# Optimization experiments

Hardware: AMD Instinct MI355X
Metric: run time of the kernel (lower is better)

## Reference

```python
import jax, jax.numpy as jnp
import numpy as np

N_HEADS = 8

def setup_inputs() -> dict:
    key = jax.random.key(0)
    ks = jax.random.split(key, 7)
    B, S, D = 4, 2048, 512
    s = 1.0 / np.sqrt(D)
    return {
        "input_Q": jax.random.normal(ks[0], (B, S, D), jnp.float32),
        "input_K": jax.random.normal(ks[1], (B, S, D), jnp.float32),
        "input_V": jax.random.normal(ks[2], (B, S, D), jnp.float32),
        "W_Q": jax.random.normal(ks[3], (D, D), jnp.float32) * s,
        "W_K": jax.random.normal(ks[4], (D, D), jnp.float32) * s,
        "W_V": jax.random.normal(ks[5], (D, D), jnp.float32) * s,
        "W_O": jax.random.normal(ks[6], (D, D), jnp.float32) * s,
    }

def reference(input_Q, input_K, input_V, W_Q, W_K, W_V, W_O):
    B, Sq, D = input_Q.shape
    Sk = input_K.shape[1]
    H = N_HEADS
    d_k = D // H
    # torch nn.Linear(bias=False): y = x @ W.T
    def proj(x, W):
        return (x @ W.T).reshape(B, -1, H, d_k).transpose(0, 2, 1, 3)  # [B,H,S,dk]
    Q = proj(input_Q, W_Q)
    K = proj(input_K, W_K)
    V = proj(input_V, W_V)
    scale = 1.0 / jnp.sqrt(jnp.float32(d_k))
    scores = jnp.einsum("bhqd,bhkd->bhqk", Q, K) * scale  # [B,H,Sq,Sk]
    # TriangularCausalMask: mask strict upper triangle with -inf
    causal = jnp.tril(jnp.ones((Sq, Sk), dtype=bool))
    scores = jnp.where(causal[None, None], scores, -jnp.inf)
    attn = jax.nn.softmax(scores, axis=-1)
    context = jnp.einsum("bhqk,bhkd->bhqd", attn, V)
    context = context.transpose(0, 2, 1, 3).reshape(B, Sq, D)
    return context @ W_O.T
```

## Files before the change

kernel.cpp:

```cpp
#include <hip/hip_runtime.h>
#include <hip/hip_bf16.h>
#include <math.h>

#define B_  4
#define S_  2048
#define D_  512
#define H_  8
#define DK_ 64
#define M_  (B_ * S_)

using bf16   = __bf16;
using bf16x4 = __bf16 __attribute__((ext_vector_type(4)));
using bf16x8 = __bf16 __attribute__((ext_vector_type(8)));
using f32x4  = float __attribute__((ext_vector_type(4)));

#define MFMA16(a, b, c) __builtin_amdgcn_mfma_f32_16x16x32_bf16((a), (b), (c), 0, 0, 0)
#define EXP2(x) exp2f(x)

typedef __attribute__((address_space(3))) void       lds_void;
typedef const __attribute__((address_space(1))) void gbl_void;

__device__ __forceinline__ void async16(const bf16* g, bf16* lds) {
    __builtin_amdgcn_global_load_lds((gbl_void*)g, (lds_void*)lds, 16, 0, 0);
}

__device__ __forceinline__ bf16x8 ldg8(const bf16* p) {
    return *reinterpret_cast<const bf16x8*>(p);
}

__device__ __forceinline__ size_t fragbase(int g, int k0, int kk, int t) {
    return ((((size_t)(g * 8 + k0) * 2 + kk) * 4 + t) * 64) * 8;
}

__global__ __launch_bounds__(256) void cvt_w(
    const float* __restrict__ w0, const float* __restrict__ w1,
    const float* __restrict__ w2, const float* __restrict__ w3,
    bf16* __restrict__ dst)
{
    const int w    = blockIdx.x * 4 + (threadIdx.x >> 6);
    const int lane = threadIdx.x & 63;
    const int lg = lane >> 4, lc = lane & 15;
    const int seg = w >> 9;
    const int c   = w & 511;
    const float* src = (seg == 0) ? w0 : (seg == 1) ? w1 : (seg == 2) ? w2 : w3;
    const size_t dbase = (size_t)seg << 18;
    const int g = c >> 6, k0 = (c >> 3) & 7, kk = (c >> 2) & 1, t = c & 3;
    const size_t soff = ((size_t)(g * 64 + t * 16 + lc) << 9) + k0 * 64 + kk * 32 + lg * 8;
    f32x4 a = *reinterpret_cast<const f32x4*>(src + soff);
    f32x4 b = *reinterpret_cast<const f32x4*>(src + soff + 4);
    bf16x8 r;
    #pragma unroll
    for (int j = 0; j < 4; ++j) { r[j] = (bf16)a[j]; r[j + 4] = (bf16)b[j]; }
    *reinterpret_cast<bf16x8*>(dst + dbase + ((size_t)c << 9) + (size_t)lane * 8) = r;
}

__global__ __launch_bounds__(256, 3) void gemm_qkv(
    const float* __restrict__ x0, const float* __restrict__ x1,
    const float* __restrict__ x2, const bf16* __restrict__ Wf,
    bf16* __restrict__ qkv)
{
    const int bx  = blockIdx.x;
    const int xcd = bx & 7;
    const int idx = bx >> 3;
    const int mt  = xcd + 8 * (idx & 7);
    const int rest = idx >> 3;
    const int nt  = rest & 3;
    const int z   = rest >> 2;

    const float* X  = (z == 0) ? x0 : (z == 1) ? x1 : x2;
    const bf16*  Wz = Wf + (size_t)z * D_ * D_;
    const bool vz = (z == 2);

    const int lane = threadIdx.x & 63;
    const int wave = threadIdx.x >> 6;
    const int lc = lane & 15;
    const int lg = lane >> 4;
    const int aIdx = wave >> 1;
    const int bIdx = wave & 1;

    __shared__ bf16 Wb[2][4096];
    __shared__ bf16 Xb[2][4096];

    const int tid  = threadIdx.x;
    const int xc   = tid >> 5;
    const int xgx  = xc >> 2, xt = xc & 3;
    const int sub  = tid & 31;
    const int l0   = 2 * sub;
    const int xrow0 = (2 * mt + xgx) * 64 + xt * 16 + (l0 & 15);
    const int xcolg = (l0 >> 4) * 8;

    auto issueX = [&](int s, f32x4* r) {
        const int col = (s >> 1) * 64 + (s & 1) * 32 + xcolg;
        const float* p0 = X + (size_t)xrow0 * 512 + col;
        r[0] = *reinterpret_cast<const f32x4*>(p0);
        r[1] = *reinterpret_cast<const f32x4*>(p0 + 4);
        r[2] = *reinterpret_cast<const f32x4*>(p0 + 512);
        r[3] = *reinterpret_cast<const f32x4*>(p0 + 516);
    };
    auto issueW = [&](int s) {
        const int k0 = s >> 1, kk = s & 1;
        bf16* wd = Wb[s & 1];
        #pragma unroll
        for (int i = 0; i < 2; ++i) {
            const int c = wave * 2 + i;
            const int gx = c >> 2, t = c & 3;
            async16(Wz + fragbase(2 * nt + gx, k0, kk, t) + (size_t)lane * 8,
                    wd + (gx * 4 + t) * 512 + (size_t)lane * 8);
        }
    };
    auto writeX = [&](int s, const f32x4* r) {
        bf16* xd = Xb[s & 1];
        bf16x8 v0, v1;
        #pragma unroll
        for (int j = 0; j < 4; ++j) {
            v0[j] = (bf16)r[0][j]; v0[j + 4] = (bf16)r[1][j];
            v1[j] = (bf16)r[2][j]; v1[j + 4] = (bf16)r[3][j];
        }
        *reinterpret_cast<bf16x8*>(xd + xc * 512 + l0 * 8)       = v0;
        *reinterpret_cast<bf16x8*>(xd + xc * 512 + (l0 + 1) * 8) = v1;
    };

    f32x4 acc[4][4] = {};

    {
        f32x4 xr[4];
        issueX(0, xr); issueW(0);
        writeX(0, xr);
        __syncthreads();
    }

    for (int s = 0; s < 16; ++s) {
        f32x4 xn[4];
        if (s < 15) { issueX(s + 1, xn); issueW(s + 1); }

        const bf16* wb = Wb[s & 1];
        const bf16* xb = Xb[s & 1];
        const bf16* ap = (vz ? xb : wb) + aIdx * 2048;
        const bf16* bp = (vz ? wb : xb) + bIdx * 2048;
        bf16x8 af[4], bfm[4];
        #pragma unroll
        for (int t = 0; t < 4; ++t) {
            af[t]  = ldg8(ap + t * 512 + (size_t)lane * 8);
            bfm[t] = ldg8(bp + t * 512 + (size_t)lane * 8);
        }
        #pragma unroll
        for (int mi = 0; mi < 4; ++mi)
            #pragma unroll
            for (int ni = 0; ni < 4; ++ni)
                acc[mi][ni] = MFMA16(af[mi], bfm[ni], acc[mi][ni]);

        if (s < 15) writeX(s + 1, xn);
        __syncthreads();
    }

    const int gA = (vz ? 2 * mt : 2 * nt) + aIdx;
    const int gB = (vz ? 2 * nt : 2 * mt) + bIdx;

    if (z < 2) {
        bf16* Y = qkv + (size_t)z * M_ * D_;
        const float sc = (z == 0) ? 0.125f * 1.4426950408889634f : 1.0f;
        #pragma unroll
        for (int mi = 0; mi < 4; ++mi)
            #pragma unroll
            for (int ni = 0; ni < 4; ++ni) {
                const int d = gA * 64 + mi * 16 + lg * 4;
                const int s = gB * 64 + ni * 16 + lc;
                bf16x4 v;
                #pragma unroll
                for (int r = 0; r < 4; ++r) v[r] = (bf16)(acc[mi][ni][r] * sc);
                const size_t oidx =
                    ((((size_t)(s >> 11) * H_ + (d >> 6)) * S_
                      + (s & (S_ - 1))) << 6) + (d & 63);
                *reinterpret_cast<bf16x4*>(&Y[oidx]) = v;
            }
    } else {
        bf16* Y = qkv + (size_t)2 * M_ * D_;
        #pragma unroll
        for (int mi = 0; mi < 4; ++mi)
            #pragma unroll
            for (int ni = 0; ni < 4; ++ni) {
                const int s = gA * 64 + mi * 16 + lg * 4;
                const int d = gB * 64 + ni * 16 + lc;
                bf16x4 v;
                #pragma unroll
                for (int r = 0; r < 4; ++r) v[r] = (bf16)acc[mi][ni][r];
                const size_t oidx =
                    ((((size_t)(s >> 11)) * H_ + (d >> 6)) << 17)
                    + (size_t)(d & 63) * S_ + (s & (S_ - 1));
                *reinterpret_cast<bf16x4*>(&Y[oidx]) = v;
            }
    }
}

__global__ __launch_bounds__(256) void gemm_out(
    const bf16* __restrict__ CtxF, const bf16* __restrict__ WoF,
    float* __restrict__ out)
{
    const int bx  = blockIdx.x;
    const int xcd = bx & 7;
    const int idx = bx >> 3;
    const int mt  = xcd + 8 * (idx & 15);
    const int nt  = idx >> 4;

    const int lane = threadIdx.x & 63;
    const int wave = threadIdx.x >> 6;
    const int lc = lane & 15;
    const int lg = lane >> 4;
    const int gA = 2 * nt + (wave >> 1);
    const int tA = (wave & 1) * 2;
    const int gB = mt;

    __shared__ bf16 Ab[3][4096];
    __shared__ bf16 Bb[3][2048];

    auto stage = [&](int s) {
        const int k0 = s >> 1, kk = s & 1;
        bf16* ad = Ab[s % 3];
        bf16* bd = Bb[s % 3];
        #pragma unroll
        for (int i = 0; i < 3; ++i) {
            const int c = wave * 3 + i;
            if (c < 8) {
                const int gx = c >> 2, t = c & 3;
                async16(WoF + fragbase(2 * nt + gx, k0, kk, t) + (size_t)lane * 8,
                        ad + (gx * 4 + t) * 512 + (size_t)lane * 8);
            } else {
                const int t = c - 8;
                async16(CtxF + fragbase(gB, k0, kk, t) + (size_t)lane * 8,
                        bd + t * 512 + (size_t)lane * 8);
            }
        }
    };

    f32x4 acc[2][4] = {};

    stage(0); stage(1);

    for (int s = 0; s < 16; ++s) {
        if (s + 1 < 16) asm volatile("s_waitcnt vmcnt(3)" ::: "memory");
        else            asm volatile("s_waitcnt vmcnt(0)" ::: "memory");
        __builtin_amdgcn_s_barrier();
        if (s + 2 < 16) stage(s + 2);

        const bf16* ab = Ab[s % 3] + (wave >> 1) * 2048;
        const bf16* bb = Bb[s % 3];
        bf16x8 af[2], bfm[4];
        #pragma unroll
        for (int ai = 0; ai < 2; ++ai)
            af[ai] = ldg8(ab + (tA + ai) * 512 + (size_t)lane * 8);
        #pragma unroll
        for (int t = 0; t < 4; ++t)
            bfm[t] = ldg8(bb + t * 512 + (size_t)lane * 8);
        #pragma unroll
        for (int ai = 0; ai < 2; ++ai)
            #pragma unroll
            for (int ni = 0; ni < 4; ++ni)
                acc[ai][ni] = MFMA16(af[ai], bfm[ni], acc[ai][ni]);
    }

    #pragma unroll
    for (int ai = 0; ai < 2; ++ai)
        #pragma unroll
        for (int ni = 0; ni < 4; ++ni) {
            const int d = gA * 64 + (tA + ai) * 16 + lg * 4;
            const int s = gB * 64 + ni * 16 + lc;
            *reinterpret_cast<f32x4*>(&out[(size_t)s * D_ + d]) = acc[ai][ni];
        }
}

__device__ __forceinline__ bf16x8 pfrag(const f32x4 a, const f32x4 b) {
    union U4 { bf16x4 v; unsigned int u[2]; };
    U4 pa, pb;
    #pragma unroll
    for (int r = 0; r < 4; ++r) { pa.v[r] = (bf16)a[r]; pb.v[r] = (bf16)b[r]; }
    auto r0 = __builtin_amdgcn_permlane16_swap(pa.u[0], pb.u[0], false, false);
    auto r1 = __builtin_amdgcn_permlane16_swap(pa.u[1], pb.u[1], false, false);
    union U8 { unsigned int u[4]; bf16x8 v; } out;
    out.u[0] = r0[0]; out.u[1] = r1[0]; out.u[2] = r0[1]; out.u[3] = r1[1];
    return out.v;
}

__global__ __launch_bounds__(512, 4) void attn(
    const bf16* __restrict__ QKV, bf16* __restrict__ CtxF)
{
    const int bx = blockIdx.x;
    const int bh = (bx & 7) * 4 + ((bx >> 3) & 3);
    const int pi = bx >> 5;
    const int b = bh >> 3, h = bh & 7;
    const size_t plane = (size_t)S_ * DK_;
    const bf16* Q  = QKV + (size_t)bh * plane;
    const bf16* Kp = QKV + (size_t)(B_ * H_) * plane + (size_t)bh * plane;
    const bf16* Vt = QKV + 2 * (size_t)(B_ * H_) * plane + (size_t)bh * plane;

    const int lane = threadIdx.x & 63;
    const int wave = threadIdx.x >> 6;
    const int wv   = wave & 3;
    const int half = wave >> 2;
    const int lc = lane & 15;
    const int lg = lane >> 4;
    const int sg = ((lg & 1) << 1) | (lg >> 1);
    const int srow = wv * 16 + lc;
    const int mrow = wv * 16 + lc;

    __shared__ bf16 Ks[4][64 * 64];
    __shared__ bf16 Vs[4][64 * 64];

    const int lo = pi;
    const int hi = 31 - pi;
    const int myq = half ? lo : hi;

    const int qR = myq * 64 + mrow;
    bf16x8 qf0 = ldg8(Q + (size_t)qR * DK_ + lg * 8);
    bf16x8 qf1 = ldg8(Q + (size_t)qR * DK_ + 32 + lg * 8);

    f32x4 accO[4] = {};
    float li = 0.f;

    auto stage = [&](int n) {
        const int kn = n * 64;
        if (half == 0) {
            bf16* kd = Ks[n & 3];
            #pragma unroll
            for (int i = 0; i < 2; ++i) {
                const int kc = i * 4 + lg;
                async16(Kp + (size_t)(kn + srow) * DK_ + kc * 8,
                        kd + (i * 256 + wv * 64) * 8);
            }
        } else {
            bf16* vd = Vs[n & 3];
            #pragma unroll
            for (int i = 0; i < 2; ++i) {
                const int kcv = i * 4 + sg;
                async16(Vt + (size_t)srow * S_ + kn + kcv * 8,
                        vd + (i * 256 + wv * 64) * 8);
            }
        }
    };

    stage(0); stage(1); stage(2);

    for (int j = 0; j <= hi; ++j) {
        if (j + 2 <= hi)      asm volatile("s_waitcnt vmcnt(4)" ::: "memory");
        else if (j + 1 <= hi) asm volatile("s_waitcnt vmcnt(2)" ::: "memory");
        else                  asm volatile("s_waitcnt vmcnt(0)" ::: "memory");
        __builtin_amdgcn_s_barrier();
        if (j + 3 <= hi) stage(j + 3);

        if (j <= myq) {
            const bf16* ks = Ks[j & 3];
            const bf16* vs = Vs[j & 3];

            bf16x8 kf0[4], kf1[4], vf0[4], vf1[4];
            #pragma unroll
            for (int t = 0; t < 4; ++t) {
                kf0[t] = ldg8(&ks[(t * 64 + lane) * 8]);
                kf1[t] = ldg8(&ks[(256 + t * 64 + lane) * 8]);
                vf0[t] = ldg8(&vs[(t * 64 + lane) * 8]);
                vf1[t] = ldg8(&vs[(256 + t * 64 + lane) * 8]);
            }

            f32x4 st[4];
            #pragma unroll
            for (int t = 0; t < 4; ++t) {
                f32x4 zz = {};
                zz = MFMA16(kf0[t], qf0, zz);
                st[t] = MFMA16(kf1[t], qf1, zz);
            }
            float rs = 0.f;
            if (j == myq) {
                #pragma unroll
                for (int t = 0; t < 4; ++t)
                    #pragma unroll
                    for (int r = 0; r < 4; ++r) {
                        const int kl = t * 16 + lg * 4 + r;
                        const float pv = EXP2((kl <= mrow) ? st[t][r] : -1e30f);
                        st[t][r] = pv;
                        rs += pv;
                    }
            } else {
                #pragma unroll
                for (int t = 0; t < 4; ++t)
                    #pragma unroll
                    for (int r = 0; r < 4; ++r) {
                        const float pv = EXP2(st[t][r]);
                        st[t][r] = pv;
                        rs += pv;
                    }
            }
            li += rs;

            const bf16x8 p0 = pfrag(st[0], st[1]);
            const bf16x8 p1 = pfrag(st[2], st[3]);

            #pragma unroll
            for (int t = 0; t < 4; ++t) {
                accO[t] = MFMA16(vf0[t], p0, accO[t]);
                accO[t] = MFMA16(vf1[t], p1, accO[t]);
            }
        }
    }

    li += __shfl_xor(li, 16); li += __shfl_xor(li, 32);
    const float rl = 1.0f / li;
    __syncthreads();
    bf16* T = &Ks[0][0] + wave * 1280;

    #pragma unroll
    for (int t = 0; t < 4; ++t) {
        bf16x4 ov;
        #pragma unroll
        for (int r = 0; r < 4; ++r) ov[r] = (bf16)(accO[t][r] * rl);
        *reinterpret_cast<bf16x4*>(&T[lc * 72 + t * 16 + lg * 4]) = ov;
    }
    #pragma unroll
    for (int kk = 0; kk < 2; ++kk) {
        bf16x8 o8 = ldg8(&T[lc * 72 + kk * 32 + lg * 8]);
        *reinterpret_cast<bf16x8*>(
            &CtxF[fragbase(b * 32 + myq, h, kk, wv) + (size_t)lane * 8]) = o8;
    }
}

extern "C" void kernel_launch(void* const* d_in, const int* in_sizes, int n_in,
                              void* d_out, int out_size, void* d_ws, size_t ws_size,
                              hipStream_t stream)
{
    float* out = (float*)d_out;

    bf16* Wf   = (bf16*)d_ws;
    bf16* qkv  = Wf + (size_t)4 * D_ * D_;
    bf16* ctxF = qkv + (size_t)3 * M_ * D_;

    cvt_w<<<512, 256, 0, stream>>>(
        (const float*)d_in[3], (const float*)d_in[4],
        (const float*)d_in[5], (const float*)d_in[6], Wf);

    gemm_qkv<<<dim3(768), 256, 0, stream>>>(
        (const float*)d_in[0], (const float*)d_in[1], (const float*)d_in[2],
        Wf, qkv);

    attn<<<dim3(512), 512, 0, stream>>>(qkv, ctxF);
    gemm_out<<<dim3(512), 256, 0, stream>>>(ctxF, Wf + (size_t)3 * D_ * D_, out);
}
```

Measured before the change: 181.9 us.

## Load QKV weight fragments directly from global and deepen X prefetch

The QKV projection GEMM stops staging weight tiles through LDS and has each wave load its pre-fragmented bf16 weight fragments straight from global memory into registers. The X prefetch is deepened to two stages in registers, the k-loop is fully unrolled, and the barrier is replaced by a custom LDS-only wait plus s_barrier. The launch-bounds occupancy hint is dropped. This aims to cut LDS traffic and async-copy latency, at the cost of more registers, global load latency on the critical path, and possibly lower occupancy.

```diff
diff --git a/kernel.cpp b/kernel.cpp
--- a/kernel.cpp
+++ b/kernel.cpp
@@ -54,7 +54,7 @@
     *reinterpret_cast<bf16x8*>(dst + dbase + ((size_t)c << 9) + (size_t)lane * 8) = r;
 }
 
-__global__ __launch_bounds__(256, 3) void gemm_qkv(
+__global__ __launch_bounds__(256) void gemm_qkv(
     const float* __restrict__ x0, const float* __restrict__ x1,
     const float* __restrict__ x2, const bf16* __restrict__ Wf,
     bf16* __restrict__ qkv)
@@ -77,8 +77,9 @@
     const int lg = lane >> 4;
     const int aIdx = wave >> 1;
     const int bIdx = wave & 1;
-
-    __shared__ bf16 Wb[2][4096];
+    const int wg = vz ? bIdx : aIdx;
+    const int xg = vz ? aIdx : bIdx;
+
     __shared__ bf16 Xb[2][4096];
 
     const int tid  = threadIdx.x;
@@ -97,17 +98,6 @@
         r[2] = *reinterpret_cast<const f32x4*>(p0 + 512);
         r[3] = *reinterpret_cast<const f32x4*>(p0 + 516);
     };
-    auto issueW = [&](int s) {
-        const int k0 = s >> 1, kk = s & 1;
-        bf16* wd = Wb[s & 1];
-        #pragma unroll
-        for (int i = 0; i < 2; ++i) {
-            const int c = wave * 2 + i;
-            const int gx = c >> 2, t = c & 3;
-            async16(Wz + fragbase(2 * nt + gx, k0, kk, t) + (size_t)lane * 8,
-                    wd + (gx * 4 + t) * 512 + (size_t)lane * 8);
-        }
-    };
     auto writeX = [&](int s, const f32x4* r) {
         bf16* xd = Xb[s & 1];
         bf16x8 v0, v1;
@@ -119,38 +109,49 @@
         *reinterpret_cast<bf16x8*>(xd + xc * 512 + l0 * 8)       = v0;
         *reinterpret_cast<bf16x8*>(xd + xc * 512 + (l0 + 1) * 8) = v1;
     };
+    auto bar = [&]() {
+        asm volatile("s_waitcnt lgkmcnt(0)" ::: "memory");
+        __builtin_amdgcn_s_barrier();
+    };
 
     f32x4 acc[4][4] = {};
-
-    {
-        f32x4 xr[4];
-        issueX(0, xr); issueW(0);
-        writeX(0, xr);
-        __syncthreads();
-    }
-
+    f32x4 xr[2][4];
+
+    issueX(0, xr[0]);
+    issueX(1, xr[1]);
+    writeX(0, xr[0]);
+    bar();
+
+    #pragma unroll
     for (int s = 0; s < 16; ++s) {
-        f32x4 xn[4];
-        if (s < 15) { issueX(s + 1, xn); issueW(s + 1); }
-
-        const bf16* wb = Wb[s & 1];
+        if (s + 2 < 16) issueX(s + 2, xr[s & 1]);
+
+        const int k0 = s >> 1, kk = s & 1;
         const bf16* xb = Xb[s & 1];
-        const bf16* ap = (vz ? xb : wb) + aIdx * 2048;
-        const bf16* bp = (vz ? wb : xb) + bIdx * 2048;
-        bf16x8 af[4], bfm[4];
-        #pragma unroll
-        for (int t = 0; t < 4; ++t) {
-            af[t]  = ldg8(ap + t * 512 + (size_t)lane * 8);
-            bfm[t] = ldg8(bp + t * 512 + (size_t)lane * 8);
-        }
-        #pragma unroll
-        for (int mi = 0; mi < 4; ++mi)
-            #pragma unroll
-            for (int ni = 0; ni < 4; ++ni)
-                acc[mi][ni] = MFMA16(af[mi], bfm[ni], acc[mi][ni]);
-
-        if (s < 15) writeX(s + 1, xn);
-        __syncthreads();
+        bf16x8 wfr[4], xfr[4];
+        #pragma unroll
+        for (int t = 0; t < 4; ++t)
+            wfr[t] = ldg8(Wz + fragbase(2 * nt + wg, k0, kk, t) + (size_t)lane * 8);
+        #pragma unroll
+        for (int t = 0; t < 4; ++t)
+            xfr[t] = ldg8(xb + (xg * 4 + t) * 512 + (size_t)lane * 8);
+
+        if (!vz) {
+            #pragma unroll
+            for (int mi = 0; mi < 4; ++mi)
+                #pragma unroll
+                for (int ni = 0; ni < 4; ++ni)
+                    acc[mi][ni] = MFMA16(wfr[mi], xfr[ni], acc[mi][ni]);
+        } else {
+            #pragma unroll
+            for (int mi = 0; mi < 4; ++mi)
+                #pragma unroll
+                for (int ni = 0; ni < 4; ++ni)
+                    acc[mi][ni] = MFMA16(xfr[mi], wfr[ni], acc[mi][ni]);
+        }
+
+        if (s + 1 < 16) writeX(s + 1, xr[(s + 1) & 1]);
+        bar();
     }
 
     const int gA = (vz ? 2 * mt : 2 * nt) + aIdx;
```

Result: no change. 183.5 us (+0.9%).
